# Performance work log

Hardware: AMD Instinct MI355X
Metric: run time of the kernel (lower is better)

## Reference

```python
import jax, jax.numpy as jnp
import numpy as np

NUM_HEADS = 16

def setup_inputs() -> dict:
    key = jax.random.key(0)
    ks = jax.random.split(key, 3)
    B, S, D = 2, 2048, 1024
    x = jax.random.normal(ks[0], (B, S, D), dtype=jnp.float32)
    # xavier-uniform style scaling for weights
    Wqkv = jax.random.normal(ks[1], (3 * D, D), dtype=jnp.float32) * (1.0 / jnp.sqrt(D))
    bqkv = jnp.zeros((3 * D,), dtype=jnp.float32)
    Wo = jax.random.normal(ks[2], (D, D), dtype=jnp.float32) * (1.0 / jnp.sqrt(D))
    bo = jnp.zeros((D,), dtype=jnp.float32)
    return {"x": x, "Wqkv": Wqkv, "bqkv": bqkv, "Wo": Wo, "bo": bo}

def reference(x, Wqkv, bqkv, Wo, bo):
    B, S, D = x.shape
    H = NUM_HEADS
    hd = D // H
    # qkv projection (torch Linear: x @ W.T + b)
    qkv = x @ Wqkv.T + bqkv                      # [B, S, 3D]
    qkv = qkv.reshape(B, S, H, 3 * hd).transpose(0, 2, 1, 3)  # [B, H, S, 3hd]
    q, k, v = jnp.split(qkv, 3, axis=-1)         # each [B, H, S, hd]
    scale = 1.0 / jnp.sqrt(jnp.asarray(hd, dtype=x.dtype))
    logits = jnp.einsum('bhqd,bhkd->bhqk', q, k) * scale  # [B, H, S, S]
    attn = jax.nn.softmax(logits, axis=-1)
    vals = jnp.einsum('bhqk,bhkd->bhqd', attn, v)         # [B, H, S, hd]
    vals = vals.transpose(0, 2, 1, 3).reshape(B, S, D)
    return vals @ Wo.T + bo
```

## Files before the change

kernel.cpp:

```cpp
#include <hip/hip_runtime.h>


typedef short short8 __attribute__((ext_vector_type(8)));
typedef unsigned short ushort8v __attribute__((ext_vector_type(8)));
typedef unsigned short ushort4v __attribute__((ext_vector_type(4)));
typedef float floatx4 __attribute__((ext_vector_type(4)));

#define S_LEN 2048
#define D_MODEL 1024
#define N_HEADS 16
#define HEAD_DIM 64

#define EXP2F(x) __builtin_amdgcn_exp2f(x)

__device__ inline float bf2f(unsigned int u16) {
    union { unsigned int i; float f; } v; v.i = u16 << 16; return v.f;
}
__device__ inline unsigned short f2b(float f) {
    union { float f; unsigned int u; } v; v.f = f;
    return (unsigned short)((v.u + 0x7FFFu + ((v.u >> 16) & 1u)) >> 16);
}
__device__ inline unsigned int fbits(float f) {
    union { float f; unsigned int u; } v; v.f = f; return v.u;
}
__device__ inline unsigned int pack_bf2(float lo, float hi) {
    return __byte_perm(fbits(lo) + 0x8000u, fbits(hi) + 0x8000u, 0x7632);
}

__device__ inline int key128(int c) {
    return (c & 0x63) | ((c & 0x0C) << 1) | ((c & 0x10) >> 2);
}

__device__ inline void gld_lds16(const unsigned short* g, unsigned short* lds) {
    __builtin_amdgcn_global_load_lds(
        (const __attribute__((address_space(1))) void*)g,
        (__attribute__((address_space(3))) void*)lds, 16, 0, 0);
}

__global__ __launch_bounds__(256)
void cvt3(const float* __restrict__ s0, const float* __restrict__ s1,
          const float* __restrict__ s2,
          unsigned short* __restrict__ d0, unsigned short* __restrict__ d1,
          unsigned short* __restrict__ d2,
          int n0, int n1, int n2) {
    const int total = n0 + n1 + n2;
    for (int g = blockIdx.x * blockDim.x + threadIdx.x; g < total;
         g += gridDim.x * blockDim.x) {
        const float* s; unsigned short* d; int l;
        if (g < n0)            { s = s0; d = d0; l = g; }
        else if (g < n0 + n1)  { s = s1; d = d1; l = g - n0; }
        else                   { s = s2; d = d2; l = g - n0 - n1; }
        const float4* sp = (const float4*)s + (size_t)l * 2;
        float4 f0 = sp[0], f1 = sp[1];
        ushort8v o;
        o[0] = f2b(f0.x); o[1] = f2b(f0.y); o[2] = f2b(f0.z); o[3] = f2b(f0.w);
        o[4] = f2b(f1.x); o[5] = f2b(f1.y); o[6] = f2b(f1.z); o[7] = f2b(f1.w);
        *(ushort8v*)(d + (size_t)l * 8) = o;
    }
}

__device__ inline void stage_u(const unsigned short* __restrict__ g, int ldk,
                               unsigned short* lds, int wave, int lane) {
    const int lr  = lane >> 3;
    const int csw = ((lane & 7) ^ lr) * 8;
    gld_lds16(g + (size_t)(wave * 8 + lr) * ldk + csw, lds + wave * 512);
}

#define STAGE_A(kk0, buf) do {                                                 \
    _Pragma("unroll")                                                          \
    for (int u = 0; u < 4; ++u)                                                \
        stage_u(Abase + (size_t)(u * 64) * K + (kk0), K,                       \
                &AS[buf][u * 4096], wave, lane);                               \
} while (0)
#define STAGE_B2(kk0, buf) do {                                 \
    stage_u(Bbase + (kk0),                    K, &BS[buf][0],    wave, lane);  \
    stage_u(Bbase + (size_t)64 * K + (kk0),   K, &BS[buf][4096], wave, lane);  \
} while (0)
#define STAGE_B1(kk0, buf) do {                                    \
    stage_u(Bbase + (size_t)128 * K + (kk0),  K, &BS[buf][8192], wave, lane);  \
} while (0)

#define QLDB(pBx) do {                                                         \
    _Pragma("unroll")                                                          \
    for (int nj = 0; nj < 3; ++nj) {                                           \
        bF[nj][0] = *(const short8*)((pBx) + nj * 1024 + co0);                 \
        bF[nj][1] = *(const short8*)((pBx) + nj * 1024 + co1);                 \
    }                                                                          \
} while (0)

#define QPHASE(pAx, mq, ...) do {                                              \
    short8 aF[2][2];                                                           \
    _Pragma("unroll")                                                          \
    for (int m2 = 0; m2 < 2; ++m2) {                                           \
        aF[m2][0] = *(const short8*)((pAx) + ((mq) * 2 + m2) * 1024 + co0);    \
        aF[m2][1] = *(const short8*)((pAx) + ((mq) * 2 + m2) * 1024 + co1);    \
    }                                                                          \
    __VA_ARGS__;                                                               \
    __builtin_amdgcn_s_barrier();                                              \
    __builtin_amdgcn_s_setprio(1);                                             \
    _Pragma("unroll")                                                          \
    for (int kk = 0; kk < 2; ++kk)                                             \
        _Pragma("unroll")                                                      \
        for (int m2 = 0; m2 < 2; ++m2)                                         \
            _Pragma("unroll")                                                  \
            for (int nj = 0; nj < 3; ++nj)                                     \
                acc[(mq) * 2 + m2][nj] = __builtin_amdgcn_mfma_f32_16x16x32_bf16( \
                    aF[m2][kk], bF[nj][kk], acc[(mq) * 2 + m2][nj], 0, 0, 0);  \
    __builtin_amdgcn_s_setprio(0);                                             \
    __builtin_amdgcn_s_barrier();                                              \
} while (0)

#define WAIT_VM3() asm volatile("s_waitcnt vmcnt(3)" ::: "memory")
#define WAIT_VM0() asm volatile("s_waitcnt vmcnt(0)" ::: "memory")

__global__ __launch_bounds__(512, 2)
void qkv_gemm(const unsigned short* __restrict__ x,
              const unsigned short* __restrict__ Wqkv,
              const float* __restrict__ bqkv,
              unsigned short* __restrict__ Qb,
              unsigned short* __restrict__ Kb,
              unsigned short* __restrict__ Vb) {
    __shared__ unsigned short AS[2][16384];
    __shared__ unsigned short BS[2][12288];

    const int tid  = threadIdx.x;
    const int lane = tid & 63;
    const int wave = tid >> 6;
    const int wm = wave >> 2;
    const int wn = wave & 3;
    const int r  = lane & 15, q2 = lane >> 4;
    const int K  = D_MODEL;

    const int idx = blockIdx.x;
    const int swz = (idx & 7) * 32 + (idx >> 3);
    const int mb = swz & 15, nb = swz >> 4;
    const int m0 = mb * 256, n0 = nb * 192;

    const unsigned short* Abase = x    + (size_t)m0 * K;
    const unsigned short* Bbase = Wqkv + (size_t)n0 * K;

    const int co0 = ((q2 ^ (r & 7)) * 8);
    const int co1 = (((q2 + 4) ^ (r & 7)) * 8);
    const unsigned short* pA0 = &AS[0][(wm * 128 + r) * 64];
    const unsigned short* pA1 = &AS[1][(wm * 128 + r) * 64];
    const unsigned short* pB0 = &BS[0][(wn * 48 + r) * 64];
    const unsigned short* pB1 = &BS[1][(wn * 48 + r) * 64];

    floatx4 acc[8][3] = {};
    short8 bF[3][2];

    STAGE_A(0, 0);
    STAGE_B2(0, 0); STAGE_B1(0, 0);
    STAGE_B2(64, 1); STAGE_B1(64, 1);
    WAIT_VM3();
    __builtin_amdgcn_s_barrier();

    for (int i = 0; i < 8; ++i) {
        const bool more = (i < 7);
        const int kA1 = i * 128 + 64;
        const int kT2 = i * 128 + 128;
        const int kT3 = i * 128 + 192;

        QLDB(pB0);
        QPHASE(pA0, 0, { STAGE_A(kA1, 1); });
        QPHASE(pA0, 1, { if (more) STAGE_B2(kT2, 0); });
        QPHASE(pA0, 2, { if (more) STAGE_B1(kT2, 0); });
        QPHASE(pA0, 3, {
            if (more) { WAIT_VM3(); } else { WAIT_VM0(); }
        });
        QLDB(pB1);
        QPHASE(pA1, 0, { if (more) STAGE_A(kT2, 0); });
        QPHASE(pA1, 1, { if (more) STAGE_B2(kT3, 1); });
        QPHASE(pA1, 2, { if (more) STAGE_B1(kT3, 1); });
        QPHASE(pA1, 3, {
            if (more) { WAIT_VM3(); }
        });
    }

#pragma unroll
    for (int mi = 0; mi < 8; mi++) {
#pragma unroll
        for (int nj = 0; nj < 3; nj++) {
            int rem = wn * 48 + nj * 16 + r;
            int n = n0 + rem;
            int typ = rem >> 6;
            int d = rem & 63;
            float bv = bqkv[n];
            int m = m0 + wm * 128 + mi * 16 + q2 * 4;
            int b = m >> 11, s = m & 2047;
            if (typ == 2) {
                ushort4v pk;
#pragma unroll
                for (int rg = 0; rg < 4; rg++) pk[rg] = f2b(acc[mi][nj][rg] + bv);
                *(ushort4v*)(Vb + ((size_t)((b * N_HEADS + nb) * HEAD_DIM + d)) * S_LEN + s) = pk;
            } else {
                unsigned short* dst = (typ == 0) ? Qb : Kb;
                float sc = (typ == 0) ? 0.180336880f : 1.0f;
#pragma unroll
                for (int rg = 0; rg < 4; rg++)
                    dst[(((size_t)(b * N_HEADS + nb)) * S_LEN + s + rg) * HEAD_DIM + d] =
                        f2b((acc[mi][nj][rg] + bv) * sc);
            }
        }
    }
}

__global__ __launch_bounds__(256)
void out_gemm(const unsigned short* __restrict__ vals,
              const unsigned short* __restrict__ Wo,
              const float* __restrict__ bo,
              float* __restrict__ out) {
    __shared__ unsigned short As[2][8192];
    __shared__ unsigned short Bs[2][8192];

    const int tid  = threadIdx.x;
    const int lane = tid & 63;
    const int wave = tid >> 6;
    const int wm = wave >> 1, wn = wave & 1;
    const int r = lane & 15, q2 = lane >> 4;
    const int K = D_MODEL;
    const int m0 = blockIdx.y * 128;
    const int n0 = blockIdx.x * 128;

    const unsigned short* Abase = vals + (size_t)m0 * K;
    const unsigned short* Bbase = Wo   + (size_t)n0 * K;

    const int lr  = lane >> 3;
    const int csw = ((lane & 7) ^ lr) * 8;

    const int co0 = ((q2 ^ (r & 7)) * 8);
    const int co1 = (((q2 + 4) ^ (r & 7)) * 8);

    floatx4 acc[4][4] = {};

#define OSTAGE(gbase, k0, lds) do {                                            \
    _Pragma("unroll")                                                          \
    for (int u = 0; u < 4; ++u)                                                \
        gld_lds16((gbase) + (size_t)(u * 32 + wave * 8 + lr) * K + (k0) + csw, \
                  (lds) + u * 2048 + wave * 512);                              \
} while (0)

    OSTAGE(Abase, 0, &As[0][0]);
    OSTAGE(Bbase, 0, &Bs[0][0]);
    __builtin_amdgcn_s_waitcnt(0);
    __syncthreads();

    int buf = 0;
    for (int k0 = 0; k0 < K; k0 += 64) {
        const bool more = (k0 + 64 < K);
        if (more) {
            OSTAGE(Abase, k0 + 64, &As[buf ^ 1][0]);
            OSTAGE(Bbase, k0 + 64, &Bs[buf ^ 1][0]);
        }
#pragma unroll
        for (int kk = 0; kk < 2; kk++) {
            const int co = kk ? co1 : co0;
            short8 aF[4], bF[4];
#pragma unroll
            for (int t = 0; t < 4; t++)
                aF[t] = *(const short8*)(&As[buf][(wm * 64 + t * 16 + r) * 64] + co);
#pragma unroll
            for (int t = 0; t < 4; t++)
                bF[t] = *(const short8*)(&Bs[buf][(wn * 64 + t * 16 + r) * 64] + co);
#pragma unroll
            for (int i = 0; i < 4; i++)
#pragma unroll
                for (int j = 0; j < 4; j++)
                    acc[i][j] = __builtin_amdgcn_mfma_f32_16x16x32_bf16(aF[i], bF[j], acc[i][j], 0, 0, 0);
        }
        if (more) {
            __builtin_amdgcn_s_waitcnt(0);
            __syncthreads();
            buf ^= 1;
        }
    }
#undef OSTAGE

#pragma unroll
    for (int i = 0; i < 4; i++) {
#pragma unroll
        for (int j = 0; j < 4; j++) {
            int n = n0 + wn * 64 + j * 16 + r;
            float bv = bo[n];
#pragma unroll
            for (int rg = 0; rg < 4; rg++) {
                int m = m0 + wm * 64 + i * 16 + q2 * 4 + rg;
                out[(size_t)m * D_MODEL + n] = acc[i][j][rg] + bv;
            }
        }
    }
}

__global__ __launch_bounds__(256, 2)
void attn_kernel(const unsigned short* __restrict__ Qb,
                 const unsigned short* __restrict__ Kb,
                 const unsigned short* __restrict__ Vg,
                 unsigned short* __restrict__ vals) {
    __shared__ unsigned short Ks[2 * 128 * 64];
    __shared__ unsigned short Vts[2 * 128 * 64];

    const int tid = threadIdx.x;
    const int lane = tid & 63;
    const int wave = tid >> 6;
    const int r = lane & 15, q2 = lane >> 4;
    const int r7 = r & 7;
    const int w32 = wave * 32;

    const int idx  = blockIdx.x;
    const int xcd  = idx & 7;
    const int slot = idx >> 3;
    const int bh   = (xcd << 2) | (slot >> 4);
    const int q0   = (slot & 15) * 128;
    const int b = bh >> 4, h = bh & 15;

    const unsigned short* Qp = Qb + (size_t)bh * S_LEN * HEAD_DIM;
    const unsigned short* Kp = Kb + (size_t)bh * S_LEN * HEAD_DIM;
    const unsigned short* Vp = Vg + (size_t)bh * HEAD_DIM * S_LEN;

    const int srow = lane >> 3;
    const int scol = ((lane & 7) ^ srow) * 8;

    int krow[4], vd[4], vpan[4];
#pragma unroll
    for (int t = 0; t < 4; t++) {
        int c = wave * 32 + t * 8 + srow;
        krow[t] = key128(c);
        vpan[t] = c >> 6;
        vd[t]   = c & 63;
    }

    {
        const int qrow = tid >> 1;
        const int c0 = (tid & 1) * 4;
#pragma unroll
        for (int cc = 0; cc < 4; cc++) {
            int cb = c0 + cc;
            const uint4* gq = (const uint4*)(Qp + (size_t)(q0 + qrow) * HEAD_DIM + cb * 8);
            *(uint4*)(Ks + qrow * 64 + ((cb ^ (qrow & 7)) * 8)) = *gq;
        }
    }
    __syncthreads();
    short8 qf[2][2];
#pragma unroll
    for (int nt = 0; nt < 2; nt++)
#pragma unroll
        for (int ks = 0; ks < 2; ks++) {
            int cb = ks * 4 + q2;
            qf[nt][ks] = *(const short8*)(Ks + (w32 + nt * 16 + r) * 64 + ((cb ^ r7) * 8));
        }
    __syncthreads();

#pragma unroll
    for (int t = 0; t < 4; t++) {
        gld_lds16(Kp + (size_t)krow[t] * HEAD_DIM + scol,
                  Ks + (wave * 32 + t * 8) * 64);
        gld_lds16(Vp + (size_t)vd[t] * S_LEN + vpan[t] * 64 + scol,
                  Vts + (wave * 32 + t * 8) * 64);
    }
    __builtin_amdgcn_s_waitcnt(0);
    __syncthreads();

    union { unsigned int u[4]; short8 s; } onesu;
    onesu.u[0] = 0x3F803F80u; onesu.u[1] = 0x3F803F80u;
    onesu.u[2] = 0x3F803F80u; onesu.u[3] = 0x3F803F80u;
    const short8 onesf = onesu.s;

    floatx4 l_acc[2] = {};
    floatx4 o_acc[2][4] = {};
    int cur = 0;

    for (int kt = 0; kt < S_LEN; kt += 128) {
        const int more = (kt + 128 < S_LEN);
        if (more) {
            const int nxt = (cur ^ 1) * 8192;
#pragma unroll
            for (int t = 0; t < 4; t++) {
                gld_lds16(Kp + (size_t)(kt + 128 + krow[t]) * HEAD_DIM + scol,
                          Ks + nxt + (wave * 32 + t * 8) * 64);
                gld_lds16(Vp + (size_t)vd[t] * S_LEN + kt + 128 + vpan[t] * 64 + scol,
                          Vts + nxt + (wave * 32 + t * 8) * 64);
            }
        }
        const int co = cur * 8192;

        floatx4 sp[8][2] = {};
        __builtin_amdgcn_s_setprio(1);
#pragma unroll
        for (int mt = 0; mt < 8; mt++)
#pragma unroll
            for (int ks = 0; ks < 2; ks++) {
                int cb = ks * 4 + q2;
                short8 kfr = *(const short8*)(Ks + co + (mt * 16 + r) * 64 + ((cb ^ r7) * 8));
#pragma unroll
                for (int nt = 0; nt < 2; nt++)
                    sp[mt][nt] = __builtin_amdgcn_mfma_f32_16x16x32_bf16(kfr, qf[nt][ks], sp[mt][nt], 0, 0, 0);
            }
        __builtin_amdgcn_s_setprio(0);

#pragma unroll
        for (int nt = 0; nt < 2; nt++)
#pragma unroll
            for (int mt = 0; mt < 8; mt++)
#pragma unroll
                for (int reg = 0; reg < 4; reg++)
                    sp[mt][nt][reg] = EXP2F(sp[mt][nt][reg]);

        short8 pa[2][4];
#pragma unroll
        for (int nt = 0; nt < 2; nt++)
#pragma unroll
            for (int ks = 0; ks < 4; ks++) {
                union { unsigned int u[4]; short8 s; } tw;
                tw.u[0] = pack_bf2(sp[2 * ks][nt][0],     sp[2 * ks][nt][1]);
                tw.u[1] = pack_bf2(sp[2 * ks][nt][2],     sp[2 * ks][nt][3]);
                tw.u[2] = pack_bf2(sp[2 * ks + 1][nt][0], sp[2 * ks + 1][nt][1]);
                tw.u[3] = pack_bf2(sp[2 * ks + 1][nt][2], sp[2 * ks + 1][nt][3]);
                pa[nt][ks] = tw.s;
            }

        __builtin_amdgcn_s_setprio(1);
#pragma unroll
        for (int dt = 0; dt < 4; dt++) {
            short8 vf[4];
#pragma unroll
            for (int ks = 0; ks < 4; ks++) {
                int cb = (ks & 1) * 4 + q2;
                vf[ks] = *(const short8*)(Vts + co + (ks >> 1) * 4096 + (dt * 16 + r) * 64 + ((cb ^ r7) * 8));
            }
#pragma unroll
            for (int nt = 0; nt < 2; nt++)
#pragma unroll
                for (int ks = 0; ks < 4; ks++)
                    o_acc[nt][dt] = __builtin_amdgcn_mfma_f32_16x16x32_bf16(pa[nt][ks], vf[ks], o_acc[nt][dt], 0, 0, 0);
        }
#pragma unroll
        for (int nt = 0; nt < 2; nt++)
#pragma unroll
            for (int ks = 0; ks < 4; ks++)
                l_acc[nt] = __builtin_amdgcn_mfma_f32_16x16x32_bf16(pa[nt][ks], onesf, l_acc[nt], 0, 0, 0);
        __builtin_amdgcn_s_setprio(0);

        if (more) {
            __builtin_amdgcn_s_waitcnt(0);
            __syncthreads();
            cur ^= 1;
        }
    }

#pragma unroll
    for (int nt = 0; nt < 2; nt++) {
#pragma unroll
        for (int reg = 0; reg < 4; reg++) {
            float inv = 1.0f / l_acc[nt][reg];
            int srow2 = q0 + w32 + nt * 16 + q2 * 4 + reg;
            size_t base = ((size_t)b * S_LEN + srow2) * D_MODEL + h * HEAD_DIM + r;
#pragma unroll
            for (int dt = 0; dt < 4; dt++)
                vals[base + dt * 16] = f2b(o_acc[nt][dt][reg] * inv);
        }
    }
}

extern "C" void kernel_launch(void* const* d_in, const int* in_sizes, int n_in,
                              void* d_out, int out_size, void* d_ws, size_t ws_size,
                              hipStream_t stream) {
    const float* x    = (const float*)d_in[0];
    const float* Wqkv = (const float*)d_in[1];
    const float* bqkv = (const float*)d_in[2];
    const float* Wo   = (const float*)d_in[3];
    const float* bo   = (const float*)d_in[4];
    float* out = (float*)d_out;

    const size_t NX = 4194304, NW = 3145728, NO = 1048576;
    unsigned short* xb    = (unsigned short*)d_ws;
    unsigned short* Wqkvb = xb + NX;
    unsigned short* Wob   = Wqkvb + NW;
    unsigned short* Qb    = Wob + NO;
    unsigned short* Kb    = Qb + NX;
    unsigned short* Vb    = Kb + NX;
    unsigned short* vals  = xb;

    cvt3<<<4096, 256, 0, stream>>>(x, Wqkv, Wo, xb, Wqkvb, Wob,
                                   (int)(NX / 8), (int)(NW / 8), (int)(NO / 8));
    qkv_gemm<<<256, 512, 0, stream>>>(xb, Wqkvb, bqkv, Qb, Kb, Vb);
    attn_kernel<<<512, 256, 0, stream>>>(Qb, Kb, Vb, vals);
    out_gemm<<<dim3(8, 32), 256, 0, stream>>>(vals, Wob, bo, out);
}
```

Before: 176.5 us.

## Split attention keys across waves with 64-query blocks and LDS reduction

The attention kernel now gives each block 64 queries instead of 128 and launches twice as many blocks. Each wave owns a 32-key slice of every 128-key tile and all 64 queries, rather than 32 queries against all keys. Row sums are accumulated in scalar lanes in place of the ones-MFMA, and partial outputs and sums are reduced across waves through LDS at the end. The aim is more parallelism and less redundant K/V fragment loading per wave, at the cost of more O accumulators and an end-of-kernel LDS reduction done serially by wave 0.

```diff
diff --git a/kernel.cpp b/kernel.cpp
--- a/kernel.cpp
+++ b/kernel.cpp
@@ -227,7 +227,6 @@
 
     const int lr  = lane >> 3;
     const int csw = ((lane & 7) ^ lr) * 8;
-
     const int co0 = ((q2 ^ (r & 7)) * 8);
     const int co1 = (((q2 + 4) ^ (r & 7)) * 8);
 
@@ -296,8 +295,9 @@
                  const unsigned short* __restrict__ Kb,
                  const unsigned short* __restrict__ Vg,
                  unsigned short* __restrict__ vals) {
-    __shared__ unsigned short Ks[2 * 128 * 64];
-    __shared__ unsigned short Vts[2 * 128 * 64];
+    __shared__ unsigned short SMEM[32768];
+    unsigned short* Ks  = SMEM;
+    unsigned short* Vts = SMEM + 16384;
 
     const int tid = threadIdx.x;
     const int lane = tid & 63;
@@ -309,8 +309,8 @@
     const int idx  = blockIdx.x;
     const int xcd  = idx & 7;
     const int slot = idx >> 3;
-    const int bh   = (xcd << 2) | (slot >> 4);
-    const int q0   = (slot & 15) * 128;
+    const int bh   = (xcd << 2) | (slot >> 5);
+    const int q0   = (slot & 31) * 64;
     const int b = bh >> 4, h = bh & 15;
 
     const unsigned short* Qp = Qb + (size_t)bh * S_LEN * HEAD_DIM;
@@ -323,50 +323,36 @@
     int krow[4], vd[4], vpan[4];
 #pragma unroll
     for (int t = 0; t < 4; t++) {
-        int c = wave * 32 + t * 8 + srow;
-        krow[t] = key128(c);
-        vpan[t] = c >> 6;
-        vd[t]   = c & 63;
-    }
-
-    {
-        const int qrow = tid >> 1;
-        const int c0 = (tid & 1) * 4;
-#pragma unroll
-        for (int cc = 0; cc < 4; cc++) {
-            int cb = c0 + cc;
-            const uint4* gq = (const uint4*)(Qp + (size_t)(q0 + qrow) * HEAD_DIM + cb * 8);
-            *(uint4*)(Ks + qrow * 64 + ((cb ^ (qrow & 7)) * 8)) = *gq;
-        }
-    }
-    __syncthreads();
-    short8 qf[2][2];
-#pragma unroll
-    for (int nt = 0; nt < 2; nt++)
-#pragma unroll
-        for (int ks = 0; ks < 2; ks++) {
-            int cb = ks * 4 + q2;
-            qf[nt][ks] = *(const short8*)(Ks + (w32 + nt * 16 + r) * 64 + ((cb ^ r7) * 8));
-        }
-    __syncthreads();
+        int c = t * 8 + srow;
+        krow[t] = w32 + key128(c);
+        int u = wave * 32 + t * 8 + srow;
+        vpan[t] = u >> 6;
+        vd[t]   = u & 63;
+    }
+
+    short8 qf[4][2];
+#pragma unroll
+    for (int qb = 0; qb < 4; qb++)
+#pragma unroll
+        for (int kk = 0; kk < 2; kk++)
+            qf[qb][kk] = *(const short8*)(
+                Qp + (size_t)(q0 + qb * 16 + r) * HEAD_DIM + kk * 32 + q2 * 8);
 
 #pragma unroll
     for (int t = 0; t < 4; t++) {
         gld_lds16(Kp + (size_t)krow[t] * HEAD_DIM + scol,
-                  Ks + (wave * 32 + t * 8) * 64);
+                  Ks + (w32 + t * 8) * 64);
         gld_lds16(Vp + (size_t)vd[t] * S_LEN + vpan[t] * 64 + scol,
                   Vts + (wave * 32 + t * 8) * 64);
     }
     __builtin_amdgcn_s_waitcnt(0);
     __syncthreads();
 
-    union { unsigned int u[4]; short8 s; } onesu;
-    onesu.u[0] = 0x3F803F80u; onesu.u[1] = 0x3F803F80u;
-    onesu.u[2] = 0x3F803F80u; onesu.u[3] = 0x3F803F80u;
-    const short8 onesf = onesu.s;
-
-    floatx4 l_acc[2] = {};
-    floatx4 o_acc[2][4] = {};
+    const int cbv = (wave & 1) * 4 + q2;
+    const int vpo = (wave >> 1) * 4096;
+
+    float l_lane[4] = {};
+    floatx4 o_acc[4][4] = {};
     int cur = 0;
 
     for (int kt = 0; kt < S_LEN; kt += 128) {
@@ -376,68 +362,58 @@
 #pragma unroll
             for (int t = 0; t < 4; t++) {
                 gld_lds16(Kp + (size_t)(kt + 128 + krow[t]) * HEAD_DIM + scol,
-                          Ks + nxt + (wave * 32 + t * 8) * 64);
+                          Ks + nxt + (w32 + t * 8) * 64);
                 gld_lds16(Vp + (size_t)vd[t] * S_LEN + kt + 128 + vpan[t] * 64 + scol,
                           Vts + nxt + (wave * 32 + t * 8) * 64);
             }
         }
         const int co = cur * 8192;
 
-        floatx4 sp[8][2] = {};
+        floatx4 sp[2][4] = {};
         __builtin_amdgcn_s_setprio(1);
 #pragma unroll
-        for (int mt = 0; mt < 8; mt++)
-#pragma unroll
-            for (int ks = 0; ks < 2; ks++) {
-                int cb = ks * 4 + q2;
-                short8 kfr = *(const short8*)(Ks + co + (mt * 16 + r) * 64 + ((cb ^ r7) * 8));
-#pragma unroll
-                for (int nt = 0; nt < 2; nt++)
-                    sp[mt][nt] = __builtin_amdgcn_mfma_f32_16x16x32_bf16(kfr, qf[nt][ks], sp[mt][nt], 0, 0, 0);
+        for (int kb = 0; kb < 2; kb++)
+#pragma unroll
+            for (int kk = 0; kk < 2; kk++) {
+                short8 kfr = *(const short8*)(
+                    Ks + co + (w32 + kb * 16 + r) * 64 + (((kk * 4 + q2) ^ r7) * 8));
+#pragma unroll
+                for (int qb = 0; qb < 4; qb++)
+                    sp[kb][qb] = __builtin_amdgcn_mfma_f32_16x16x32_bf16(kfr, qf[qb][kk], sp[kb][qb], 0, 0, 0);
             }
         __builtin_amdgcn_s_setprio(0);
 
 #pragma unroll
-        for (int nt = 0; nt < 2; nt++)
-#pragma unroll
-            for (int mt = 0; mt < 8; mt++)
-#pragma unroll
-                for (int reg = 0; reg < 4; reg++)
-                    sp[mt][nt][reg] = EXP2F(sp[mt][nt][reg]);
-
-        short8 pa[2][4];
-#pragma unroll
-        for (int nt = 0; nt < 2; nt++)
-#pragma unroll
-            for (int ks = 0; ks < 4; ks++) {
-                union { unsigned int u[4]; short8 s; } tw;
-                tw.u[0] = pack_bf2(sp[2 * ks][nt][0],     sp[2 * ks][nt][1]);
-                tw.u[1] = pack_bf2(sp[2 * ks][nt][2],     sp[2 * ks][nt][3]);
-                tw.u[2] = pack_bf2(sp[2 * ks + 1][nt][0], sp[2 * ks + 1][nt][1]);
-                tw.u[3] = pack_bf2(sp[2 * ks + 1][nt][2], sp[2 * ks + 1][nt][3]);
-                pa[nt][ks] = tw.s;
-            }
+        for (int qb = 0; qb < 4; qb++)
+#pragma unroll
+            for (int kb = 0; kb < 2; kb++)
+#pragma unroll
+                for (int reg = 0; reg < 4; reg++) {
+                    float e = EXP2F(sp[kb][qb][reg]);
+                    sp[kb][qb][reg] = e;
+                    l_lane[qb] += e;
+                }
+
+        short8 pa[4];
+#pragma unroll
+        for (int qb = 0; qb < 4; qb++) {
+            union { unsigned int u[4]; short8 s; } tw;
+            tw.u[0] = pack_bf2(sp[0][qb][0], sp[0][qb][1]);
+            tw.u[1] = pack_bf2(sp[0][qb][2], sp[0][qb][3]);
+            tw.u[2] = pack_bf2(sp[1][qb][0], sp[1][qb][1]);
+            tw.u[3] = pack_bf2(sp[1][qb][2], sp[1][qb][3]);
+            pa[qb] = tw.s;
+        }
 
         __builtin_amdgcn_s_setprio(1);
 #pragma unroll
         for (int dt = 0; dt < 4; dt++) {
-            short8 vf[4];
-#pragma unroll
-            for (int ks = 0; ks < 4; ks++) {
-                int cb = (ks & 1) * 4 + q2;
-                vf[ks] = *(const short8*)(Vts + co + (ks >> 1) * 4096 + (dt * 16 + r) * 64 + ((cb ^ r7) * 8));
-            }
-#pragma unroll
-            for (int nt = 0; nt < 2; nt++)
-#pragma unroll
-                for (int ks = 0; ks < 4; ks++)
-                    o_acc[nt][dt] = __builtin_amdgcn_mfma_f32_16x16x32_bf16(pa[nt][ks], vf[ks], o_acc[nt][dt], 0, 0, 0);
-        }
-#pragma unroll
-        for (int nt = 0; nt < 2; nt++)
-#pragma unroll
-            for (int ks = 0; ks < 4; ks++)
-                l_acc[nt] = __builtin_amdgcn_mfma_f32_16x16x32_bf16(pa[nt][ks], onesf, l_acc[nt], 0, 0, 0);
+            short8 vf = *(const short8*)(
+                Vts + co + vpo + (dt * 16 + r) * 64 + ((cbv ^ r7) * 8));
+#pragma unroll
+            for (int qb = 0; qb < 4; qb++)
+                o_acc[qb][dt] = __builtin_amdgcn_mfma_f32_16x16x32_bf16(pa[qb], vf, o_acc[qb][dt], 0, 0, 0);
+        }
         __builtin_amdgcn_s_setprio(0);
 
         if (more) {
@@ -448,15 +424,48 @@
     }
 
 #pragma unroll
-    for (int nt = 0; nt < 2; nt++) {
-#pragma unroll
-        for (int reg = 0; reg < 4; reg++) {
-            float inv = 1.0f / l_acc[nt][reg];
-            int srow2 = q0 + w32 + nt * 16 + q2 * 4 + reg;
-            size_t base = ((size_t)b * S_LEN + srow2) * D_MODEL + h * HEAD_DIM + r;
+    for (int qb = 0; qb < 4; qb++) {
+        l_lane[qb] += __shfl_xor(l_lane[qb], 16, 64);
+        l_lane[qb] += __shfl_xor(l_lane[qb], 32, 64);
+    }
+
+    __syncthreads();
+    float* lred = (float*)SMEM;
+    float* ored = (float*)SMEM + 256;
+    if (q2 == 0) {
+#pragma unroll
+        for (int qb = 0; qb < 4; qb++)
+            lred[wave * 64 + qb * 16 + r] = l_lane[qb];
+    }
+    if (wave != 0) {
+        float* my = ored + (wave - 1) * 4096;
+#pragma unroll
+        for (int qb = 0; qb < 4; qb++)
 #pragma unroll
             for (int dt = 0; dt < 4; dt++)
-                vals[base + dt * 16] = f2b(o_acc[nt][dt][reg] * inv);
+#pragma unroll
+                for (int reg = 0; reg < 4; reg++)
+                    my[(qb * 16 + q2 * 4 + reg) * 64 + dt * 16 + r] = o_acc[qb][dt][reg];
+    }
+    __syncthreads();
+
+    if (wave == 0) {
+#pragma unroll
+        for (int qb = 0; qb < 4; qb++) {
+#pragma unroll
+            for (int reg = 0; reg < 4; reg++) {
+                int q = qb * 16 + q2 * 4 + reg;
+                float lsum = lred[q] + lred[64 + q] + lred[128 + q] + lred[192 + q];
+                float inv = 1.0f / lsum;
+                int srow2 = q0 + q;
+                size_t base = ((size_t)b * S_LEN + srow2) * D_MODEL + h * HEAD_DIM + r;
+#pragma unroll
+                for (int dt = 0; dt < 4; dt++) {
+                    int od = q * 64 + dt * 16 + r;
+                    float v = o_acc[qb][dt][reg] + ored[od] + ored[4096 + od] + ored[8192 + od];
+                    vals[base + dt * 16] = f2b(v * inv);
+                }
+            }
         }
     }
 }
@@ -483,6 +492,6 @@
     cvt3<<<4096, 256, 0, stream>>>(x, Wqkv, Wo, xb, Wqkvb, Wob,
                                    (int)(NX / 8), (int)(NW / 8), (int)(NO / 8));
     qkv_gemm<<<256, 512, 0, stream>>>(xb, Wqkvb, bqkv, Qb, Kb, Vb);
-    attn_kernel<<<512, 256, 0, stream>>>(Qb, Kb, Vb, vals);
+    attn_kernel<<<1024, 256, 0, stream>>>(Qb, Kb, Vb, vals);
     out_gemm<<<dim3(8, 32), 256, 0, stream>>>(vals, Wob, bo, out);
 }
```

Measured after the change: 187.2 us. 6.0% more time.
